# Performance work log

Hardware: AMD Instinct MI355X
Metric: run time of the kernel (lower is better)

The kernel has to match this reference:

```python
import jax, jax.numpy as jnp
import numpy as np

INPUT_DIM = 512
HIDDEN_DIM = 1024
N, L = 128, 512


def setup_inputs() -> dict:
    key = jax.random.key(0)
    ks = jax.random.split(key, 17)
    d = {"X": jax.random.normal(ks[0], (N, L, INPUT_DIM), dtype=jnp.float32)}
    bd = 1.0 / np.sqrt(HIDDEN_DIM)
    for gi, g in enumerate(["i", "f", "g", "o"]):
        d[f"lam_{g}"] = jax.random.normal(ks[1 + 4 * gi], (HIDDEN_DIM,), dtype=jnp.float32) * 0.02
        d[f"binv_{g}"] = jnp.zeros((HIDDEN_DIM,), dtype=jnp.float32)
        d[f"W_{g}"] = jax.random.uniform(ks[2 + 4 * gi], (HIDDEN_DIM, HIDDEN_DIM), dtype=jnp.float32, minval=-bd, maxval=bd)
        d[f"b_{g}"] = jax.random.uniform(ks[3 + 4 * gi], (HIDDEN_DIM,), dtype=jnp.float32, minval=-bd, maxval=bd)
    return d


def reference(X, lam_i, binv_i, W_i, b_i, lam_f, binv_f, W_f, b_f,
              lam_g, binv_g, W_g, b_g, lam_o, binv_o, W_o, b_o):
    # G-invariant layer (DeepSets invariant): y = lambda * sum_over_features(x) + b
    s = jnp.sum(X, axis=-1, keepdims=True)           # (N, L, 1)
    pre_i = s * lam_i + binv_i                       # (N, L, H)
    pre_f = s * lam_f + binv_f
    pre_g = s * lam_g + binv_g
    pre_o = s * lam_o + binv_o
    # time-major for scan: (L, N, H)
    xs = (jnp.swapaxes(pre_i, 0, 1), jnp.swapaxes(pre_f, 0, 1),
          jnp.swapaxes(pre_g, 0, 1), jnp.swapaxes(pre_o, 0, 1))
    n = X.shape[0]
    h0 = jnp.zeros((n, HIDDEN_DIM), dtype=X.dtype)
    c0 = jnp.zeros((n, HIDDEN_DIM), dtype=X.dtype)

    def step(carry, inp):
        h, c = carry
        pi, pf, pg, po = inp
        i = jax.nn.sigmoid(pi + h @ W_i.T + b_i)
        f = jax.nn.sigmoid(pf + h @ W_f.T + b_f)
        g = jax.nn.sigmoid(pg + h @ W_g.T + b_g)   # note: sigmoid, as in source
        o = jax.nn.sigmoid(po + h @ W_o.T + b_o)
        c_new = f * c + i * g                      # at t=0, c=0 => i*g, matching source
        h_new = o * jax.nn.sigmoid(c_new)          # c activation is sigmoid in source
        return (h_new, c_new), h_new

    _, out = jax.lax.scan(step, (h0, c0), xs)       # out: (L, N, H)
    return jnp.swapaxes(out, 0, 1)                  # (N, L, H)
```

## Files before the change

### kernel.cpp

```cpp
#include <hip/hip_runtime.h>
#include <cstdint>
#include <cstddef>

#define NN 128
#define LL 512
#define DD 512
#define HH 1024
#define NJ 4096
#define ASTR 1024
#define BSTR 1024
#define NCH 4

#define AHI 0
#define BHI 8192
#define BUFS 24576

typedef __attribute__((ext_vector_type(8))) _Float16 half8;
typedef __attribute__((ext_vector_type(4))) float f32x4;

__device__ __forceinline__ unsigned short f2h(float x) {
  union { _Float16 h; unsigned short u; } v; v.h = (_Float16)x; return v.u;
}
__device__ __forceinline__ float sigf(float x) { return 1.0f / (1.0f + __expf(-x)); }

__device__ __forceinline__ void glds16(const void* g, const void* l) {
  __builtin_amdgcn_global_load_lds(
      (const __attribute__((address_space(1))) unsigned int*)g,
      (__attribute__((address_space(3))) unsigned int*)l, 16, 0, 0);
}

__global__ __launch_bounds__(256)
void sum_rows_kernel(const float* __restrict__ X, float* __restrict__ sT) {
  int row  = blockIdx.x * 4 + (threadIdx.x >> 6);
  int lane = threadIdx.x & 63;
  const float* x = X + (size_t)row * DD + lane * 8;
  float4 a = *(const float4*)x;
  float4 b = *(const float4*)(x + 4);
  float v = (a.x + a.y) + (a.z + a.w) + (b.x + b.y) + (b.z + b.w);
#pragma unroll
  for (int off = 32; off > 0; off >>= 1) v += __shfl_down(v, off, 64);
  if (lane == 0) {
    int n = row >> 9, l = row & 511;
    sT[l * NN + n] = v;
  }
}

__global__ __launch_bounds__(256)
void wpack_kernel(const float* __restrict__ Wi, const float* __restrict__ Wf,
                  const float* __restrict__ Wg, const float* __restrict__ Wo,
                  unsigned short* __restrict__ B) {
  int idx = blockIdx.x * 256 + threadIdx.x;
  int j = idx >> 7;
  int k = (idx & 127) << 3;
  int hc = j >> 2, g = j & 3;
  const float* W = (g == 0) ? Wi : (g == 1) ? Wf : (g == 2) ? Wg : Wo;
  const float4 x0 = *(const float4*)(W + (size_t)hc * HH + k);
  const float4 x1 = *(const float4*)(W + (size_t)hc * HH + k + 4);
  float xv[8] = {x0.x, x0.y, x0.z, x0.w, x1.x, x1.y, x1.z, x1.w};
  unsigned short* d = B + (size_t)j * BSTR + k;
#pragma unroll
  for (int e = 0; e < 8; ++e) d[e] = f2h(xv[e]);
}

__global__ __launch_bounds__(256)
void pack_kernel(const float* li, const float* lf, const float* lg, const float* lo_,
                 const float* bvi, const float* bvf, const float* bvg, const float* bvo,
                 const float* bi, const float* bf_, const float* bg, const float* bo,
                 float* __restrict__ lamP, float* __restrict__ biasP) {
  int j = blockIdx.x * 256 + threadIdx.x;
  int hc = j >> 2, g = j & 3;
  const float* lam = (g == 0) ? li : (g == 1) ? lf : (g == 2) ? lg : lo_;
  const float* bv  = (g == 0) ? bvi : (g == 1) ? bvf : (g == 2) ? bvg : bvo;
  const float* bb  = (g == 0) ? bi : (g == 1) ? bf_ : (g == 2) ? bg : bo;
  lamP[j] = lam[hc];
  biasP[j] = bv[hc] + bb[hc];
}

__global__ __launch_bounds__(256)
void t0_kernel(const float* __restrict__ sT, const float* __restrict__ lamP,
               const float* __restrict__ biasP, float* __restrict__ out,
               float* __restrict__ cbuf, unsigned short* __restrict__ A0) {
  int id = blockIdx.x * 256 + threadIdx.x;
  int n = id >> 10, hc = id & 1023;
  float sv = sT[n];
  float4 lam = *(const float4*)(lamP + 4 * hc);
  float4 bia = *(const float4*)(biasP + 4 * hc);
  float vi = sigf(sv * lam.x + bia.x);
  float vg = sigf(sv * lam.z + bia.z);
  float vo = sigf(sv * lam.w + bia.w);
  float cn = vi * vg;
  float hn = vo * sigf(cn);
  cbuf[n * HH + hc] = cn;
  out[(size_t)n * (LL * HH) + hc] = hn;
  A0[(size_t)n * ASTR + hc] = f2h(hn);
}

__global__ __launch_bounds__(256, 1)
void step_kernel(const unsigned short* __restrict__ Aprev,
                 const unsigned short* __restrict__ Bbuf,
                 const float* __restrict__ sT, const float* __restrict__ lamP,
                 const float* __restrict__ biasP, float* __restrict__ out,
                 float* __restrict__ cbuf, unsigned short* __restrict__ Acur, int t)
{
  __shared__ alignas(16) short lds[2][BUFS];

  const int tid = threadIdx.x;
  const int ln  = tid & 63;
  const int w   = tid >> 6;

  const int bid = blockIdx.x;
  const int wl  = (bid & 7) * 32 + (bid >> 3);
  const int Nt  = wl >> 2;
  const int Mt  = wl & 3;
  const int n0  = Mt * 32;
  const int j0  = Nt * 64;

  const char* srcb[12];
  int ldsoff[12];
  {
    const int ps = ln & 15;
    const int rr = ln >> 4;
#pragma unroll
    for (int i = 0; i < 12; ++i) {
      int sub = i >= 6;
      int p = w * 6 + (i - sub * 6);
      const char* s; int off;
      if (p < 8)  { int r = p * 4 + rr;       int sp = (ps & 8) | ((ps ^ r) & 7);
                    s = (const char*)(Aprev + (size_t)(n0 + r) * ASTR + sub * 128 + sp * 8);
                    off = AHI + sub * 4096 + p * 512; }
      else        { int pb = p - 8;  int r = pb * 4 + rr;
                    int sp = (ps & 8) | ((ps ^ r) & 7);
                    s = (const char*)(Bbuf + (size_t)(j0 + r) * BSTR + sub * 128 + sp * 8);
                    off = BHI + sub * 8192 + pb * 512; }
      srcb[i] = s; ldsoff[i] = off;
    }
  }

  int aoff[2][8], boff[8];
  {
    const int hs = ln >> 4;
#pragma unroll
    for (int sl = 0; sl < 8; ++sl) {
      int sub = sl >> 2;
      int s   = (sl & 3) * 4 + hs;
#pragma unroll
      for (int mf = 0; mf < 2; ++mf) {
        int rA = mf * 16 + (ln & 15);
        aoff[mf][sl] = AHI + sub * 4096 + rA * 128 + (((s & 8) | ((s ^ rA) & 7)) << 3);
      }
      int rB = w * 16 + (ln & 15);
      boff[sl] = BHI + sub * 8192 + rB * 128 + (((s & 8) | ((s ^ rB) & 7)) << 3);
    }
  }

  const int jj = j0 + w * 16 + (ln & 15);
  const float lamv = lamP[jj];
  const float biav = biasP[jj];
  const int rbase = (ln >> 4) * 4;
  const int hc = jj >> 2;
  float cold[2][4], svp[2][4];
#pragma unroll
  for (int mf = 0; mf < 2; ++mf)
#pragma unroll
    for (int r = 0; r < 4; ++r) {
      const int m = n0 + mf * 16 + rbase + r;
      cold[mf][r] = cbuf[m * HH + hc];
      svp[mf][r]  = sT[t * NN + m];
    }

  f32x4 acc0 = {0.f,0.f,0.f,0.f};
  f32x4 acc1 = {0.f,0.f,0.f,0.f};

  auto stage = [&](int c, int b) {
    const int co = c * 512;
#pragma unroll
    for (int i = 0; i < 12; ++i) glds16(srcb[i] + co, &lds[b][ldsoff[i]]);
  };

  stage(0, 0);
#pragma unroll
  for (int c = 0; c < NCH; ++c) {
    const int b = c & 1;
    __builtin_amdgcn_s_barrier();
    if (c < NCH - 1) {
      stage(c + 1, b ^ 1);
      asm volatile("s_waitcnt vmcnt(12)" ::: "memory");
    } else {
      asm volatile("s_waitcnt vmcnt(0)" ::: "memory");
    }
    __builtin_amdgcn_s_barrier();
#pragma unroll
    for (int sl = 0; sl < 8; ++sl) {
      half8 a0 = *(const half8*)&lds[b][aoff[0][sl]];
      half8 a1 = *(const half8*)&lds[b][aoff[1][sl]];
      half8 bb = *(const half8*)&lds[b][boff[sl]];
      acc0 = __builtin_amdgcn_mfma_f32_16x16x32_f16(a0, bb, acc0, 0, 0, 0);
      acc1 = __builtin_amdgcn_mfma_f32_16x16x32_f16(a1, bb, acc1, 0, 0, 0);
    }
  }

#pragma unroll
  for (int mf = 0; mf < 2; ++mf) {
    const int m0 = n0 + mf * 16 + rbase;
#pragma unroll
    for (int r = 0; r < 4; ++r) {
      const int m = m0 + r;
      float a = (mf == 0) ? acc0[r] : acc1[r];
      float v = sigf(a + svp[mf][r] * lamv + biav);
      const int base = ln & ~3;
      float vi = __shfl(v, base + 0, 64);
      float vf = __shfl(v, base + 1, 64);
      float vg = __shfl(v, base + 2, 64);
      float vo = __shfl(v, base + 3, 64);
      if ((ln & 3) == 0) {
        float cn = vf * cold[mf][r] + vi * vg;
        float hn = vo * sigf(cn);
        cbuf[m * HH + hc] = cn;
        out[(size_t)m * (LL * HH) + (size_t)t * HH + hc] = hn;
        Acur[(size_t)m * ASTR + hc] = f2h(hn);
      }
    }
  }
}

extern "C" void kernel_launch(void* const* d_in, const int* in_sizes, int n_in,
                              void* d_out, int out_size, void* d_ws, size_t ws_size,
                              hipStream_t stream) {
  const float* X    = (const float*)d_in[0];
  const float* lami = (const float*)d_in[1];
  const float* bvi  = (const float*)d_in[2];
  const float* Wi   = (const float*)d_in[3];
  const float* bi   = (const float*)d_in[4];
  const float* lamf = (const float*)d_in[5];
  const float* bvf  = (const float*)d_in[6];
  const float* Wf   = (const float*)d_in[7];
  const float* bf_  = (const float*)d_in[8];
  const float* lamg = (const float*)d_in[9];
  const float* bvg  = (const float*)d_in[10];
  const float* Wg   = (const float*)d_in[11];
  const float* bg   = (const float*)d_in[12];
  const float* lamo = (const float*)d_in[13];
  const float* bvo  = (const float*)d_in[14];
  const float* Wo   = (const float*)d_in[15];
  const float* bo   = (const float*)d_in[16];

  float* out  = (float*)d_out;

  float* cbuf  = (float*)d_ws;
  float* sT    = cbuf + (size_t)NN * HH;
  float* lamP  = sT + (size_t)NN * LL;
  float* biasP = lamP + NJ;
  unsigned short* A0 = (unsigned short*)(biasP + NJ);
  unsigned short* A1 = A0 + (size_t)NN * ASTR;
  unsigned short* Bb = A1 + (size_t)NN * ASTR;

  sum_rows_kernel<<<(NN * LL) / 4, 256, 0, stream>>>(X, sT);
  wpack_kernel<<<(NJ * 128) / 256, 256, 0, stream>>>(Wi, Wf, Wg, Wo, Bb);
  pack_kernel<<<NJ / 256, 256, 0, stream>>>(lami, lamf, lamg, lamo,
                                            bvi, bvf, bvg, bvo,
                                            bi, bf_, bg, bo, lamP, biasP);
  t0_kernel<<<(NN * HH) / 256, 256, 0, stream>>>(sT, lamP, biasP, out, cbuf, A0);

  for (int t = 1; t < LL; ++t) {
    const unsigned short* Ap = (t & 1) ? A0 : A1;
    unsigned short* Ac = (t & 1) ? (unsigned short*)A1 : A0;
    step_kernel<<<256, 256, 0, stream>>>(Ap, Bb, sT, lamP, biasP, out, cbuf, Ac, t);
  }
}
```

Before: 3.564 ms.

## Load weight fragments directly into registers and halve step-kernel tile to 32 columns

Each step block now covers 32 packed gate columns with 2 wavefronts, launched as 512 blocks of 128 threads instead of 256 blocks of 256 threads. The B (weight) operand is read straight from global memory into double-buffered registers rather than staged through LDS, so LDS holds only the A (hidden-state) tile. The aim is to cut LDS traffic and footprint, raise occupancy, and spread the latency-bound per-timestep GEMM across more CUs. The cost is higher register pressure and uncoalesced 16-byte global reads of the weights on every step, with the vmcnt wait count retuned by hand.

New measurement: 4.450 ms. 1.25x slower.

```diff
diff --git a/kernel.cpp b/kernel.cpp
--- a/kernel.cpp
+++ b/kernel.cpp
@@ -10,10 +10,6 @@
 #define ASTR 1024
 #define BSTR 1024
 #define NCH 4
-
-#define AHI 0
-#define BHI 8192
-#define BUFS 24576
 
 typedef __attribute__((ext_vector_type(8))) _Float16 half8;
 typedef __attribute__((ext_vector_type(4))) float f32x4;
@@ -95,63 +91,56 @@
   A0[(size_t)n * ASTR + hc] = f2h(hn);
 }
 
-__global__ __launch_bounds__(256, 1)
+__global__ __launch_bounds__(128, 2)
 void step_kernel(const unsigned short* __restrict__ Aprev,
                  const unsigned short* __restrict__ Bbuf,
                  const float* __restrict__ sT, const float* __restrict__ lamP,
                  const float* __restrict__ biasP, float* __restrict__ out,
                  float* __restrict__ cbuf, unsigned short* __restrict__ Acur, int t)
 {
-  __shared__ alignas(16) short lds[2][BUFS];
+  __shared__ alignas(16) short lds[2][8192];
 
   const int tid = threadIdx.x;
   const int ln  = tid & 63;
   const int w   = tid >> 6;
 
   const int bid = blockIdx.x;
-  const int wl  = (bid & 7) * 32 + (bid >> 3);
+  const int wl  = (bid & 7) * 64 + (bid >> 3);
   const int Nt  = wl >> 2;
   const int Mt  = wl & 3;
   const int n0  = Mt * 32;
-  const int j0  = Nt * 64;
-
-  const char* srcb[12];
-  int ldsoff[12];
-  {
-    const int ps = ln & 15;
-    const int rr = ln >> 4;
-#pragma unroll
-    for (int i = 0; i < 12; ++i) {
-      int sub = i >= 6;
-      int p = w * 6 + (i - sub * 6);
-      const char* s; int off;
-      if (p < 8)  { int r = p * 4 + rr;       int sp = (ps & 8) | ((ps ^ r) & 7);
-                    s = (const char*)(Aprev + (size_t)(n0 + r) * ASTR + sub * 128 + sp * 8);
-                    off = AHI + sub * 4096 + p * 512; }
-      else        { int pb = p - 8;  int r = pb * 4 + rr;
-                    int sp = (ps & 8) | ((ps ^ r) & 7);
-                    s = (const char*)(Bbuf + (size_t)(j0 + r) * BSTR + sub * 128 + sp * 8);
-                    off = BHI + sub * 8192 + pb * 512; }
-      srcb[i] = s; ldsoff[i] = off;
-    }
-  }
-
-  int aoff[2][8], boff[8];
-  {
-    const int hs = ln >> 4;
-#pragma unroll
-    for (int sl = 0; sl < 8; ++sl) {
-      int sub = sl >> 2;
-      int s   = (sl & 3) * 4 + hs;
-#pragma unroll
-      for (int mf = 0; mf < 2; ++mf) {
-        int rA = mf * 16 + (ln & 15);
-        aoff[mf][sl] = AHI + sub * 4096 + rA * 128 + (((s & 8) | ((s ^ rA) & 7)) << 3);
-      }
-      int rB = w * 16 + (ln & 15);
-      boff[sl] = BHI + sub * 8192 + rB * 128 + (((s & 8) | ((s ^ rB) & 7)) << 3);
-    }
-  }
+  const int j0  = Nt * 32;
+
+  const int ps = ln & 15;
+  const int rr = ln >> 4;
+  const int hs8 = (ln >> 4) * 8;
+
+  const char* srcb[8];
+  int ldsoff[8];
+#pragma unroll
+  for (int i = 0; i < 8; ++i) {
+    int p = w * 8 + i;
+    int sub = p >> 3;
+    int pr  = p & 7;
+    int r   = pr * 4 + rr;
+    int sp  = (ps & 8) | ((ps ^ r) & 7);
+    srcb[i] = (const char*)(Aprev + (size_t)(n0 + r) * ASTR + sub * 128 + sp * 8);
+    ldsoff[i] = sub * 4096 + pr * 512;
+  }
+
+  int aoff[2][8];
+#pragma unroll
+  for (int sl = 0; sl < 8; ++sl) {
+    int sub = sl >> 2;
+    int s   = (sl & 3) * 4 + (ln >> 4);
+#pragma unroll
+    for (int mf = 0; mf < 2; ++mf) {
+      int rA = mf * 16 + (ln & 15);
+      aoff[mf][sl] = sub * 4096 + rA * 128 + (((s & 8) | ((s ^ rA) & 7)) << 3);
+    }
+  }
+
+  const unsigned short* Bp = Bbuf + (size_t)(j0 + w * 16 + (ln & 15)) * BSTR;
 
   const int jj = j0 + w * 16 + (ln & 15);
   const float lamv = lamP[jj];
@@ -170,30 +159,46 @@
 
   f32x4 acc0 = {0.f,0.f,0.f,0.f};
   f32x4 acc1 = {0.f,0.f,0.f,0.f};
-
-  auto stage = [&](int c, int b) {
-    const int co = c * 512;
-#pragma unroll
-    for (int i = 0; i < 12; ++i) glds16(srcb[i] + co, &lds[b][ldsoff[i]]);
-  };
-
-  stage(0, 0);
+  half8 brA[8], brB[8];
+
+  stageA0: ;
+#pragma unroll
+  for (int i = 0; i < 8; ++i) glds16(srcb[i], &lds[0][ldsoff[i]]);
+  __builtin_amdgcn_sched_barrier(0);
+#pragma unroll
+  for (int sl = 0; sl < 8; ++sl)
+    brA[sl] = *(const half8*)(Bp + sl * 32 + hs8);
+  __builtin_amdgcn_sched_barrier(0);
+
 #pragma unroll
   for (int c = 0; c < NCH; ++c) {
     const int b = c & 1;
     __builtin_amdgcn_s_barrier();
     if (c < NCH - 1) {
-      stage(c + 1, b ^ 1);
-      asm volatile("s_waitcnt vmcnt(12)" ::: "memory");
+      const int co = (c + 1) * 512;
+#pragma unroll
+      for (int i = 0; i < 8; ++i) glds16(srcb[i] + co, &lds[b ^ 1][ldsoff[i]]);
+      __builtin_amdgcn_sched_barrier(0);
+      const int ce = (c + 1) * 256;
+      if (b) {
+#pragma unroll
+        for (int sl = 0; sl < 8; ++sl) brA[sl] = *(const half8*)(Bp + ce + sl * 32 + hs8);
+      } else {
+#pragma unroll
+        for (int sl = 0; sl < 8; ++sl) brB[sl] = *(const half8*)(Bp + ce + sl * 32 + hs8);
+      }
+      __builtin_amdgcn_sched_barrier(0);
+      asm volatile("s_waitcnt vmcnt(16)" ::: "memory");
     } else {
       asm volatile("s_waitcnt vmcnt(0)" ::: "memory");
     }
+    __builtin_amdgcn_sched_barrier(0);
     __builtin_amdgcn_s_barrier();
 #pragma unroll
     for (int sl = 0; sl < 8; ++sl) {
       half8 a0 = *(const half8*)&lds[b][aoff[0][sl]];
       half8 a1 = *(const half8*)&lds[b][aoff[1][sl]];
-      half8 bb = *(const half8*)&lds[b][boff[sl]];
+      half8 bb = b ? brB[sl] : brA[sl];
       acc0 = __builtin_amdgcn_mfma_f32_16x16x32_f16(a0, bb, acc0, 0, 0, 0);
       acc1 = __builtin_amdgcn_mfma_f32_16x16x32_f16(a1, bb, acc1, 0, 0, 0);
     }
@@ -264,6 +269,6 @@
   for (int t = 1; t < LL; ++t) {
     const unsigned short* Ap = (t & 1) ? A0 : A1;
     unsigned short* Ac = (t & 1) ? (unsigned short*)A1 : A0;
-    step_kernel<<<256, 256, 0, stream>>>(Ap, Bb, sT, lamP, biasP, out, cbuf, Ac, t);
-  }
-}
+    step_kernel<<<512, 128, 0, stream>>>(Ap, Bb, sT, lamP, biasP, out, cbuf, Ac, t);
+  }
+}
```

## Replace per-timestep launches with persistent kernel using global flag synchronization

Applied to the files above, without the earlier changes.

Collapses 511 step-kernel launches and the t0 kernel into one persistent kernel of 256 blocks that loops over all timesteps. Each block keeps its slice of packed weights resident in LDS and the cell state in registers. Blocks wait on per-row-group flags in global memory, read with cache-bypassing loads, before consuming the previous hidden state. This removes launch overhead and repeated weight reloads, but relies on all 256 blocks being co-resident and on spin-wait correctness under the memory model.

New measurement: 4.254 ms. 19.4% more time.

```diff
diff --git a/kernel.cpp b/kernel.cpp
--- a/kernel.cpp
+++ b/kernel.cpp
@@ -11,12 +11,9 @@
 #define BSTR 1024
 #define NCH 4
 
-#define AHI 0
-#define BHI 8192
-#define BUFS 24576
-
 typedef __attribute__((ext_vector_type(8))) _Float16 half8;
 typedef __attribute__((ext_vector_type(4))) float f32x4;
+typedef __attribute__((ext_vector_type(4))) unsigned u32x4;
 
 __device__ __forceinline__ unsigned short f2h(float x) {
   union { _Float16 h; unsigned short u; } v; v.h = (_Float16)x; return v.u;
@@ -27,6 +24,29 @@
   __builtin_amdgcn_global_load_lds(
       (const __attribute__((address_space(1))) unsigned int*)g,
       (__attribute__((address_space(3))) unsigned int*)l, 16, 0, 0);
+}
+
+__device__ __forceinline__ u32x4 load16_sc(const void* p) {
+  u32x4 r;
+  asm volatile("global_load_dwordx4 %0, %1, off sc0 sc1" : "=v"(r) : "v"(p));
+  return r;
+}
+__device__ __forceinline__ void store2_sc(void* p, unsigned v) {
+  asm volatile("global_store_short %0, %1, off sc0 sc1" :: "v"(p), "v"(v) : "memory");
+}
+__device__ __forceinline__ void store4_sc(void* p, unsigned v) {
+  asm volatile("global_store_dword %0, %1, off sc0 sc1" :: "v"(p), "v"(v) : "memory");
+}
+__device__ __forceinline__ unsigned load4_sc(const void* p) {
+  unsigned r;
+  asm volatile("global_load_dword %0, %1, off sc0 sc1\n\ts_waitcnt vmcnt(0)"
+               : "=v"(r) : "v"(p) : "memory");
+  return r;
+}
+
+__global__ __launch_bounds__(256)
+void zero_flags_kernel(unsigned* __restrict__ flags) {
+  store4_sc(flags + threadIdx.x, 0u);
 }
 
 __global__ __launch_bounds__(256)
@@ -76,33 +96,18 @@
   biasP[j] = bv[hc] + bb[hc];
 }
 
-__global__ __launch_bounds__(256)
-void t0_kernel(const float* __restrict__ sT, const float* __restrict__ lamP,
-               const float* __restrict__ biasP, float* __restrict__ out,
-               float* __restrict__ cbuf, unsigned short* __restrict__ A0) {
-  int id = blockIdx.x * 256 + threadIdx.x;
-  int n = id >> 10, hc = id & 1023;
-  float sv = sT[n];
-  float4 lam = *(const float4*)(lamP + 4 * hc);
-  float4 bia = *(const float4*)(biasP + 4 * hc);
-  float vi = sigf(sv * lam.x + bia.x);
-  float vg = sigf(sv * lam.z + bia.z);
-  float vo = sigf(sv * lam.w + bia.w);
-  float cn = vi * vg;
-  float hn = vo * sigf(cn);
-  cbuf[n * HH + hc] = cn;
-  out[(size_t)n * (LL * HH) + hc] = hn;
-  A0[(size_t)n * ASTR + hc] = f2h(hn);
-}
-
 __global__ __launch_bounds__(256, 1)
-void step_kernel(const unsigned short* __restrict__ Aprev,
-                 const unsigned short* __restrict__ Bbuf,
-                 const float* __restrict__ sT, const float* __restrict__ lamP,
-                 const float* __restrict__ biasP, float* __restrict__ out,
-                 float* __restrict__ cbuf, unsigned short* __restrict__ Acur, int t)
+void persist_kernel(const unsigned short* __restrict__ Bbuf,
+                    const float* __restrict__ sT,
+                    const float* __restrict__ lamP,
+                    const float* __restrict__ biasP,
+                    float* __restrict__ out,
+                    unsigned short* __restrict__ Ag0,
+                    unsigned short* __restrict__ Ag1,
+                    unsigned* __restrict__ flags)
 {
-  __shared__ alignas(16) short lds[2][BUFS];
+  __shared__ alignas(16) short Bsm[65536];
+  __shared__ alignas(16) short Asm[8192];
 
   const int tid = threadIdx.x;
   const int ln  = tid & 63;
@@ -114,112 +119,141 @@
   const int Mt  = wl & 3;
   const int n0  = Mt * 32;
   const int j0  = Nt * 64;
-
-  const char* srcb[12];
-  int ldsoff[12];
-  {
-    const int ps = ln & 15;
-    const int rr = ln >> 4;
-#pragma unroll
-    for (int i = 0; i < 12; ++i) {
-      int sub = i >= 6;
-      int p = w * 6 + (i - sub * 6);
-      const char* s; int off;
-      if (p < 8)  { int r = p * 4 + rr;       int sp = (ps & 8) | ((ps ^ r) & 7);
-                    s = (const char*)(Aprev + (size_t)(n0 + r) * ASTR + sub * 128 + sp * 8);
-                    off = AHI + sub * 4096 + p * 512; }
-      else        { int pb = p - 8;  int r = pb * 4 + rr;
-                    int sp = (ps & 8) | ((ps ^ r) & 7);
-                    s = (const char*)(Bbuf + (size_t)(j0 + r) * BSTR + sub * 128 + sp * 8);
-                    off = BHI + sub * 8192 + pb * 512; }
-      srcb[i] = s; ldsoff[i] = off;
-    }
-  }
+  unsigned* gf = flags + Mt * 64;
+
+  const int ps = ln & 15;
+  const int rr = ln >> 4;
+
+#pragma unroll
+  for (int i = 0; i < 32; ++i) {
+    int pb = w * 32 + i;
+    int plane = pb >> 4, rg = pb & 15;
+    int r  = rg * 4 + rr;
+    int sp = (ps & 8) | ((ps ^ r) & 7);
+    glds16(Bbuf + (size_t)(j0 + r) * BSTR + plane * 128 + sp * 8,
+           &Bsm[plane * 8192 + rg * 512]);
+  }
+  asm volatile("s_waitcnt vmcnt(0)" ::: "memory");
+  __builtin_amdgcn_s_barrier();
+
+  const int ar = tid >> 3;
+  int sQ[4], dQ[4];
+#pragma unroll
+  for (int q = 0; q < 4; ++q) {
+    int s = (tid & 7) * 4 + q;
+    int sub = s >> 4, sl16 = s & 15;
+    sQ[q] = (sub * 128 + sl16 * 8) * 2;
+    dQ[q] = sub * 4096 + ar * 128 + (((sl16 & 8) | ((sl16 ^ ar) & 7)) << 3);
+  }
+  const size_t arowb = (size_t)(n0 + ar) * (ASTR * 2);
 
   int aoff[2][8], boff[8];
   {
     const int hs = ln >> 4;
 #pragma unroll
     for (int sl = 0; sl < 8; ++sl) {
-      int sub = sl >> 2;
-      int s   = (sl & 3) * 4 + hs;
+      int s = (sl & 3) * 4 + hs;
 #pragma unroll
       for (int mf = 0; mf < 2; ++mf) {
         int rA = mf * 16 + (ln & 15);
-        aoff[mf][sl] = AHI + sub * 4096 + rA * 128 + (((s & 8) | ((s ^ rA) & 7)) << 3);
+        aoff[mf][sl] = (sl >> 2) * 4096 + rA * 128 + (((s & 8) | ((s ^ rA) & 7)) << 3);
       }
       int rB = w * 16 + (ln & 15);
-      boff[sl] = BHI + sub * 8192 + rB * 128 + (((s & 8) | ((s ^ rB) & 7)) << 3);
+      boff[sl] = (sl >> 2) * 8192 + rB * 128 + (((s & 8) | ((s ^ rB) & 7)) << 3);
     }
   }
 
   const int jj = j0 + w * 16 + (ln & 15);
   const float lamv = lamP[jj];
   const float biav = biasP[jj];
-  const int rbase = (ln >> 4) * 4;
+  const int rbase = rr * 4;
   const int hc = jj >> 2;
-  float cold[2][4], svp[2][4];
-#pragma unroll
-  for (int mf = 0; mf < 2; ++mf)
-#pragma unroll
-    for (int r = 0; r < 4; ++r) {
-      const int m = n0 + mf * 16 + rbase + r;
-      cold[mf][r] = cbuf[m * HH + hc];
-      svp[mf][r]  = sT[t * NN + m];
-    }
-
-  f32x4 acc0 = {0.f,0.f,0.f,0.f};
-  f32x4 acc1 = {0.f,0.f,0.f,0.f};
-
-  auto stage = [&](int c, int b) {
-    const int co = c * 512;
-#pragma unroll
-    for (int i = 0; i < 12; ++i) glds16(srcb[i] + co, &lds[b][ldsoff[i]]);
-  };
-
-  stage(0, 0);
-#pragma unroll
-  for (int c = 0; c < NCH; ++c) {
-    const int b = c & 1;
-    __builtin_amdgcn_s_barrier();
-    if (c < NCH - 1) {
-      stage(c + 1, b ^ 1);
-      asm volatile("s_waitcnt vmcnt(12)" ::: "memory");
-    } else {
-      asm volatile("s_waitcnt vmcnt(0)" ::: "memory");
-    }
-    __builtin_amdgcn_s_barrier();
-#pragma unroll
-    for (int sl = 0; sl < 8; ++sl) {
-      half8 a0 = *(const half8*)&lds[b][aoff[0][sl]];
-      half8 a1 = *(const half8*)&lds[b][aoff[1][sl]];
-      half8 bb = *(const half8*)&lds[b][boff[sl]];
-      acc0 = __builtin_amdgcn_mfma_f32_16x16x32_f16(a0, bb, acc0, 0, 0, 0);
-      acc1 = __builtin_amdgcn_mfma_f32_16x16x32_f16(a1, bb, acc1, 0, 0, 0);
-    }
-  }
-
-#pragma unroll
-  for (int mf = 0; mf < 2; ++mf) {
-    const int m0 = n0 + mf * 16 + rbase;
-#pragma unroll
-    for (int r = 0; r < 4; ++r) {
-      const int m = m0 + r;
-      float a = (mf == 0) ? acc0[r] : acc1[r];
-      float v = sigf(a + svp[mf][r] * lamv + biav);
-      const int base = ln & ~3;
-      float vi = __shfl(v, base + 0, 64);
-      float vf = __shfl(v, base + 1, 64);
-      float vg = __shfl(v, base + 2, 64);
-      float vo = __shfl(v, base + 3, 64);
-      if ((ln & 3) == 0) {
-        float cn = vf * cold[mf][r] + vi * vg;
-        float hn = vo * sigf(cn);
-        cbuf[m * HH + hc] = cn;
-        out[(size_t)m * (LL * HH) + (size_t)t * HH + hc] = hn;
-        Acur[(size_t)m * ASTR + hc] = f2h(hn);
+  float creg[2][4] = {{0.f,0.f,0.f,0.f},{0.f,0.f,0.f,0.f}};
+
+  for (int t = 0; t < LL; ++t) {
+    unsigned short* Acur = (t & 1) ? Ag1 : Ag0;
+    f32x4 acc0 = {0.f,0.f,0.f,0.f};
+    f32x4 acc1 = {0.f,0.f,0.f,0.f};
+
+    float svp[2][4];
+#pragma unroll
+    for (int mf = 0; mf < 2; ++mf)
+#pragma unroll
+      for (int r = 0; r < 4; ++r)
+        svp[mf][r] = sT[t * NN + n0 + mf * 16 + rbase + r];
+
+    if (t > 0) {
+      const unsigned short* Ap = (t & 1) ? Ag0 : Ag1;
+
+      if (w == 0) {
+        const unsigned* fp = gf + ln;
+        for (;;) {
+          unsigned v = load4_sc(fp);
+          if (__all((int)v >= t)) break;
+          __builtin_amdgcn_s_sleep(2);
+        }
+      }
+      __builtin_amdgcn_s_barrier();
+      __builtin_amdgcn_sched_barrier(0);
+
+      u32x4 rA[4][4];
+      const char* abase = (const char*)Ap + arowb;
+#pragma unroll
+      for (int c2 = 0; c2 < 4; ++c2)
+#pragma unroll
+        for (int q = 0; q < 4; ++q)
+          rA[c2][q] = load16_sc(abase + c2 * 512 + sQ[q]);
+      __builtin_amdgcn_sched_barrier(0);
+
+#pragma unroll
+      for (int c = 0; c < NCH; ++c) {
+        if (c == 0)      asm volatile("s_waitcnt vmcnt(12)" ::: "memory");
+        else if (c == 1) asm volatile("s_waitcnt vmcnt(8)"  ::: "memory");
+        else if (c == 2) asm volatile("s_waitcnt vmcnt(4)"  ::: "memory");
+        else             asm volatile("s_waitcnt vmcnt(0)"  ::: "memory");
+        __builtin_amdgcn_sched_barrier(0);
+#pragma unroll
+        for (int q = 0; q < 4; ++q) *(u32x4*)&Asm[dQ[q]] = rA[c][q];
+        asm volatile("s_waitcnt lgkmcnt(0)" ::: "memory");
+        __builtin_amdgcn_s_barrier();
+#pragma unroll
+        for (int sl = 0; sl < 8; ++sl) {
+          half8 a0 = *(const half8*)&Asm[aoff[0][sl]];
+          half8 a1 = *(const half8*)&Asm[aoff[1][sl]];
+          half8 bb = *(const half8*)&Bsm[c * 16384 + boff[sl]];
+          acc0 = __builtin_amdgcn_mfma_f32_16x16x32_f16(a0, bb, acc0, 0, 0, 0);
+          acc1 = __builtin_amdgcn_mfma_f32_16x16x32_f16(a1, bb, acc1, 0, 0, 0);
+        }
+        __builtin_amdgcn_s_barrier();
       }
     }
+
+#pragma unroll
+    for (int mf = 0; mf < 2; ++mf) {
+      const int m0 = n0 + mf * 16 + rbase;
+#pragma unroll
+      for (int r = 0; r < 4; ++r) {
+        const int m = m0 + r;
+        float a = (mf == 0) ? acc0[r] : acc1[r];
+        float v = sigf(a + svp[mf][r] * lamv + biav);
+        const int base = ln & ~3;
+        float vi = __shfl(v, base + 0, 64);
+        float vf = __shfl(v, base + 1, 64);
+        float vg = __shfl(v, base + 2, 64);
+        float vo = __shfl(v, base + 3, 64);
+        float cn = vf * creg[mf][r] + vi * vg;
+        creg[mf][r] = cn;
+        float hn = vo * sigf(cn);
+        if ((ln & 3) == 0) {
+          out[(size_t)m * (LL * HH) + (size_t)t * HH + hc] = hn;
+          store2_sc(Acur + (size_t)m * ASTR + hc, (unsigned)f2h(hn));
+        }
+      }
+    }
+
+    asm volatile("s_waitcnt vmcnt(0)" ::: "memory");
+    __builtin_amdgcn_s_barrier();
+    if (tid == 0) store4_sc(&flags[Mt * 64 + Nt], (unsigned)(t + 1));
   }
 }
 
@@ -244,26 +278,23 @@
   const float* Wo   = (const float*)d_in[15];
   const float* bo   = (const float*)d_in[16];
 
-  float* out  = (float*)d_out;
-
-  float* cbuf  = (float*)d_ws;
-  float* sT    = cbuf + (size_t)NN * HH;
+  float* out = (float*)d_out;
+
+  float* sT    = (float*)d_ws;
   float* lamP  = sT + (size_t)NN * LL;
   float* biasP = lamP + NJ;
-  unsigned short* A0 = (unsigned short*)(biasP + NJ);
-  unsigned short* A1 = A0 + (size_t)NN * ASTR;
-  unsigned short* Bb = A1 + (size_t)NN * ASTR;
-
+  unsigned short* Ag0 = (unsigned short*)(biasP + NJ);
+  unsigned short* Ag1 = Ag0 + (size_t)NN * ASTR;
+  unsigned short* Bb  = Ag1 + (size_t)NN * ASTR;
+  unsigned* flags = (unsigned*)(Bb + (size_t)NJ * BSTR);
+
+  zero_flags_kernel<<<1, 256, 0, stream>>>(flags);
   sum_rows_kernel<<<(NN * LL) / 4, 256, 0, stream>>>(X, sT);
   wpack_kernel<<<(NJ * 128) / 256, 256, 0, stream>>>(Wi, Wf, Wg, Wo, Bb);
   pack_kernel<<<NJ / 256, 256, 0, stream>>>(lami, lamf, lamg, lamo,
                                             bvi, bvf, bvg, bvo,
                                             bi, bf_, bg, bo, lamP, biasP);
-  t0_kernel<<<(NN * HH) / 256, 256, 0, stream>>>(sT, lamP, biasP, out, cbuf, A0);
-
-  for (int t = 1; t < LL; ++t) {
-    const unsigned short* Ap = (t & 1) ? A0 : A1;
-    unsigned short* Ac = (t & 1) ? (unsigned short*)A1 : A0;
-    step_kernel<<<256, 256, 0, stream>>>(Ap, Bb, sT, lamP, biasP, out, cbuf, Ac, t);
-  }
-}
+
+  persist_kernel<<<dim3(256), dim3(256), 0, stream>>>(Bb, sT, lamP, biasP,
+                                                      out, Ag0, Ag1, flags);
+}
```

## Split step kernel into 512 smaller blocks of 128 threads with 32-column tiles

Applied to the files above, without the earlier changes.

Each recurrent step now runs 512 workgroups of two waves, each computing a 32x32 output tile instead of 32x64, so more of the 256 CUs are used and two blocks can share a CU. The LDS staging layout and load assignment are reworked so each wave issues 16 async global-to-LDS loads, and sched_barriers pin the order of loads and waits. The trade-off is that the A tile is reloaded by twice as many blocks, and each block has fewer waves to hide latency.

New measurement: 3.748 ms. +5.2%, slower.

```diff
diff --git a/kernel.cpp b/kernel.cpp
--- a/kernel.cpp
+++ b/kernel.cpp
@@ -10,10 +10,6 @@
 #define ASTR 1024
 #define BSTR 1024
 #define NCH 4
-
-#define AHI 0
-#define BHI 8192
-#define BUFS 24576
 
 typedef __attribute__((ext_vector_type(8))) _Float16 half8;
 typedef __attribute__((ext_vector_type(4))) float f32x4;
@@ -95,43 +91,49 @@
   A0[(size_t)n * ASTR + hc] = f2h(hn);
 }
 
-__global__ __launch_bounds__(256, 1)
+__global__ __launch_bounds__(128, 2)
 void step_kernel(const unsigned short* __restrict__ Aprev,
                  const unsigned short* __restrict__ Bbuf,
                  const float* __restrict__ sT, const float* __restrict__ lamP,
                  const float* __restrict__ biasP, float* __restrict__ out,
                  float* __restrict__ cbuf, unsigned short* __restrict__ Acur, int t)
 {
-  __shared__ alignas(16) short lds[2][BUFS];
+  __shared__ alignas(16) short lds[2][16384];
 
   const int tid = threadIdx.x;
   const int ln  = tid & 63;
   const int w   = tid >> 6;
 
   const int bid = blockIdx.x;
-  const int wl  = (bid & 7) * 32 + (bid >> 3);
+  const int wl  = (bid & 7) * 64 + (bid >> 3);
   const int Nt  = wl >> 2;
   const int Mt  = wl & 3;
   const int n0  = Mt * 32;
-  const int j0  = Nt * 64;
-
-  const char* srcb[12];
-  int ldsoff[12];
+  const int j0  = Nt * 32;
+
+  const char* srcb[16];
+  int ldsoff[16];
   {
     const int ps = ln & 15;
     const int rr = ln >> 4;
 #pragma unroll
-    for (int i = 0; i < 12; ++i) {
-      int sub = i >= 6;
-      int p = w * 6 + (i - sub * 6);
+    for (int i = 0; i < 16; ++i) {
+      int p = w * 16 + i;
       const char* s; int off;
-      if (p < 8)  { int r = p * 4 + rr;       int sp = (ps & 8) | ((ps ^ r) & 7);
-                    s = (const char*)(Aprev + (size_t)(n0 + r) * ASTR + sub * 128 + sp * 8);
-                    off = AHI + sub * 4096 + p * 512; }
-      else        { int pb = p - 8;  int r = pb * 4 + rr;
-                    int sp = (ps & 8) | ((ps ^ r) & 7);
-                    s = (const char*)(Bbuf + (size_t)(j0 + r) * BSTR + sub * 128 + sp * 8);
-                    off = BHI + sub * 8192 + pb * 512; }
+      if (p < 16) {
+        int sub = p >> 3, pr = p & 7;
+        int r = pr * 4 + rr;
+        int sp = (ps & 8) | ((ps ^ r) & 7);
+        s = (const char*)(Aprev + (size_t)(n0 + r) * ASTR + sub * 128 + sp * 8);
+        off = sub * 4096 + pr * 512;
+      } else {
+        int q = p - 16;
+        int sub = q >> 3, pr = q & 7;
+        int r = pr * 4 + rr;
+        int sp = (ps & 8) | ((ps ^ r) & 7);
+        s = (const char*)(Bbuf + (size_t)(j0 + r) * BSTR + sub * 128 + sp * 8);
+        off = 8192 + sub * 4096 + pr * 512;
+      }
       srcb[i] = s; ldsoff[i] = off;
     }
   }
@@ -146,10 +148,10 @@
 #pragma unroll
       for (int mf = 0; mf < 2; ++mf) {
         int rA = mf * 16 + (ln & 15);
-        aoff[mf][sl] = AHI + sub * 4096 + rA * 128 + (((s & 8) | ((s ^ rA) & 7)) << 3);
+        aoff[mf][sl] = sub * 4096 + rA * 128 + (((s & 8) | ((s ^ rA) & 7)) << 3);
       }
       int rB = w * 16 + (ln & 15);
-      boff[sl] = BHI + sub * 8192 + rB * 128 + (((s & 8) | ((s ^ rB) & 7)) << 3);
+      boff[sl] = 8192 + sub * 4096 + rB * 128 + (((s & 8) | ((s ^ rB) & 7)) << 3);
     }
   }
 
@@ -167,6 +169,7 @@
       cold[mf][r] = cbuf[m * HH + hc];
       svp[mf][r]  = sT[t * NN + m];
     }
+  __builtin_amdgcn_sched_barrier(0);
 
   f32x4 acc0 = {0.f,0.f,0.f,0.f};
   f32x4 acc1 = {0.f,0.f,0.f,0.f};
@@ -174,17 +177,19 @@
   auto stage = [&](int c, int b) {
     const int co = c * 512;
 #pragma unroll
-    for (int i = 0; i < 12; ++i) glds16(srcb[i] + co, &lds[b][ldsoff[i]]);
+    for (int i = 0; i < 16; ++i) glds16(srcb[i] + co, &lds[b][ldsoff[i]]);
   };
 
   stage(0, 0);
+  __builtin_amdgcn_sched_barrier(0);
 #pragma unroll
   for (int c = 0; c < NCH; ++c) {
     const int b = c & 1;
     __builtin_amdgcn_s_barrier();
     if (c < NCH - 1) {
       stage(c + 1, b ^ 1);
-      asm volatile("s_waitcnt vmcnt(12)" ::: "memory");
+      __builtin_amdgcn_sched_barrier(0);
+      asm volatile("s_waitcnt vmcnt(16)" ::: "memory");
     } else {
       asm volatile("s_waitcnt vmcnt(0)" ::: "memory");
     }
@@ -264,6 +269,6 @@
   for (int t = 1; t < LL; ++t) {
     const unsigned short* Ap = (t & 1) ? A0 : A1;
     unsigned short* Ac = (t & 1) ? (unsigned short*)A1 : A0;
-    step_kernel<<<256, 256, 0, stream>>>(Ap, Bb, sT, lamP, biasP, out, cbuf, Ac, t);
-  }
-}
+    step_kernel<<<512, 128, 0, stream>>>(Ap, Bb, sT, lamP, biasP, out, cbuf, Ac, t);
+  }
+}
```
